# Optimization experiments

Hardware: AMD Instinct MI355X
Metric: run time of the kernel (lower is better)

## Reference

```python
import jax, jax.numpy as jnp
import numpy as np

B, S, D = 2, 2048, 4096
H, HKV, HD = 32, 8, 128
G = H // HKV  # GQA groups
ROPE_BASE = 10000.0


def setup_inputs() -> dict:
    key = jax.random.key(0)
    kx, kq, kk, kv, ko = jax.random.split(key, 5)
    w = 0.02  # init scale for stability
    return {
        "x": jax.random.normal(kx, (B, S, D), dtype=jnp.float32),
        "Wq": jax.random.normal(kq, (D, H * HD), dtype=jnp.float32) * w,
        "Wk": jax.random.normal(kk, (D, HKV * HD), dtype=jnp.float32) * w,
        "Wv": jax.random.normal(kv, (D, HKV * HD), dtype=jnp.float32) * w,
        "Wo": jax.random.normal(ko, (H * HD, D), dtype=jnp.float32) * w,
    }


def _rope(t):
    # t: (B, h, S, HD); rotate-half RoPE, positions = arange(S)
    s = t.shape[2]
    pos = jnp.arange(s, dtype=jnp.float32)
    inv_freq = 1.0 / (ROPE_BASE ** (jnp.arange(0, HD, 2, dtype=jnp.float32) / HD))
    ang = pos[:, None] * inv_freq[None, :]            # (S, HD/2)
    cos = jnp.concatenate([jnp.cos(ang), jnp.cos(ang)], axis=-1)  # (S, HD)
    sin = jnp.concatenate([jnp.sin(ang), jnp.sin(ang)], axis=-1)
    t1, t2 = jnp.split(t, 2, axis=-1)
    rot = jnp.concatenate([-t2, t1], axis=-1)
    return t * cos.astype(t.dtype) + rot * sin.astype(t.dtype)


def reference(x, Wq, Wk, Wv, Wo):
    b, s, _ = x.shape
    q = (x @ Wq).reshape(b, s, H, HD).transpose(0, 2, 1, 3)      # (B,H,S,HD)
    k = (x @ Wk).reshape(b, s, HKV, HD).transpose(0, 2, 1, 3)    # (B,HKV,S,HD)
    v = (x @ Wv).reshape(b, s, HKV, HD).transpose(0, 2, 1, 3)
    q = _rope(q)
    k = _rope(k)
    # GQA: broadcast KV heads across groups instead of repeat_interleave
    qg = q.reshape(b, HKV, G, s, HD)
    scale = 1.0 / jnp.sqrt(jnp.asarray(HD, dtype=x.dtype))
    scores = jnp.einsum('bkgsd,bktd->bkgst', qg, k) * scale       # (B,HKV,G,S,S)
    causal = jnp.tril(jnp.ones((s, s), dtype=bool))
    scores = jnp.where(causal, scores, jnp.finfo(scores.dtype).min)
    p = jax.nn.softmax(scores, axis=-1)
    out = jnp.einsum('bkgst,bktd->bkgsd', p, v)                   # (B,HKV,G,S,HD)
    out = out.reshape(b, H, s, HD).transpose(0, 2, 1, 3).reshape(b, s, H * HD)
    return out @ Wo
```

## Files before the change

kernel.cpp:

```cpp
#include <hip/hip_runtime.h>
#include <hip/hip_bf16.h>

#define B_   2
#define S_   2048
#define D_   4096
#define H_   32
#define HKV_ 8
#define HD_  128
#define QKVS 6144

typedef __bf16 bf16;
typedef __bf16 bf16x8 __attribute__((ext_vector_type(8)));
typedef __bf16 bf16x4 __attribute__((ext_vector_type(4)));
typedef float  f32x4  __attribute__((ext_vector_type(4)));


__global__ void cast_f32_bf16_kernel(const float* __restrict__ in, bf16* __restrict__ out, int n) {
    int i = (blockIdx.x * blockDim.x + threadIdx.x) * 4;
    if (i >= n) return;
    const float4 v = *(const float4*)(in + i);
    bf16x4 o;
    o[0] = (bf16)v.x; o[1] = (bf16)v.y; o[2] = (bf16)v.z; o[3] = (bf16)v.w;
    *(bf16x4*)(out + i) = o;
}

__global__ void transpose_cast_kernel(const float* __restrict__ W, bf16* __restrict__ WT, int K, int N) {
    __shared__ float t[32][33];
    const int n0 = blockIdx.x * 32, k0 = blockIdx.y * 32;
    const int tx = threadIdx.x, ty = threadIdx.y;
    #pragma unroll
    for (int i = ty; i < 32; i += 8) t[i][tx] = W[(size_t)(k0 + i) * N + n0 + tx];
    __syncthreads();
    #pragma unroll
    for (int i = ty; i < 32; i += 8) WT[(size_t)(n0 + i) * K + k0 + tx] = (bf16)t[tx][i];
}

__global__ void transpose_v_kernel(const bf16* __restrict__ V, bf16* __restrict__ Vt) {
    __shared__ bf16 t[32][33];
    const int bh = blockIdx.z;
    const int b = bh >> 3, hk = bh & 7;
    const int d0 = blockIdx.x * 32, s0 = blockIdx.y * 32;
    const int tx = threadIdx.x, ty = threadIdx.y;
    #pragma unroll
    for (int i = ty; i < 32; i += 8)
        t[i][tx] = V[((size_t)(b * S_ + s0 + i)) * QKVS + hk * HD_ + d0 + tx];
    __syncthreads();
    #pragma unroll
    for (int i = ty; i < 32; i += 8)
        Vt[((size_t)(bh * HD_ + d0 + i)) * S_ + s0 + tx] = t[tx][i];
}

__global__ void rope_kernel(bf16* __restrict__ T, int nh, int stride) {
    const int row = blockIdx.x;
    const int pos = row & (S_ - 1);
    const size_t base = (size_t)row * stride;
    const int npairs = nh * 64;
    const float c = 13.287712379549449f / 64.0f;
    for (int p = threadIdx.x; p < npairs; p += blockDim.x) {
        const int h = p >> 6, d = p & 63;
        const float invf = exp2f(-(float)d * c);
        const float ang = (float)pos * invf;
        float sn, cs;
        sincosf(ang, &sn, &cs);
        const size_t i1 = base + (size_t)h * HD_ + d;
        const size_t i2 = i1 + 64;
        const float a  = (float)T[i1];
        const float b2 = (float)T[i2];
        T[i1] = (bf16)(a * cs - b2 * sn);
        T[i2] = (bf16)(b2 * cs + a * sn);
    }
}

__device__ __forceinline__ void gload_lds16(const bf16* g, bf16* l) {
    __builtin_amdgcn_global_load_lds((const __attribute__((address_space(1))) void*)g,
                                     (__attribute__((address_space(3))) void*)l, 16, 0, 0);
}


template <typename CT>
__global__ __launch_bounds__(256) void gemm_bt_kernel(const bf16* __restrict__ A,
                                                      const bf16* __restrict__ Bm,
                                                      CT* __restrict__ C,
                                                      int M, int Cs, int K) {
    __shared__ bf16 As[128 * 32];
    __shared__ bf16 Bs[128 * 32];
    const int m0 = blockIdx.x * 128, n0 = blockIdx.y * 128;
    const int tid = threadIdx.x;
    const int lane = tid & 63, wid = tid >> 6;
    const int wm = wid >> 1, wn = wid & 1;
    const int lg = lane >> 4, lr = lane & 15;
    f32x4 acc[4][4] = {};
    const int arow = tid >> 2;
    const int achunk = (tid & 3) * 8;
    for (int k0 = 0; k0 < K; k0 += 32) {
        gload_lds16(A  + (size_t)(m0 + arow) * K      + k0 + achunk, As + tid * 8);
        gload_lds16(A  + (size_t)(m0 + 64 + arow) * K + k0 + achunk, As + 2048 + tid * 8);
        gload_lds16(Bm + (size_t)(n0 + arow) * K      + k0 + achunk, Bs + tid * 8);
        gload_lds16(Bm + (size_t)(n0 + 64 + arow) * K + k0 + achunk, Bs + 2048 + tid * 8);
        __syncthreads();
        bf16x8 af[4], bfv[4];
        #pragma unroll
        for (int i = 0; i < 4; i++) {
            af[i]  = *(const bf16x8*)(As + (wm * 64 + i * 16 + lr) * 32 + lg * 8);
            bfv[i] = *(const bf16x8*)(Bs + (wn * 64 + i * 16 + lr) * 32 + lg * 8);
        }
        #pragma unroll
        for (int mi = 0; mi < 4; mi++)
            #pragma unroll
            for (int ni = 0; ni < 4; ni++)
                acc[mi][ni] = __builtin_amdgcn_mfma_f32_16x16x32_bf16(af[mi], bfv[ni], acc[mi][ni], 0, 0, 0);
        __syncthreads();
    }
    #pragma unroll
    for (int mi = 0; mi < 4; mi++)
        #pragma unroll
        for (int ni = 0; ni < 4; ni++)
            #pragma unroll
            for (int r = 0; r < 4; r++) {
                const int row = m0 + wm * 64 + mi * 16 + lg * 4 + r;
                const int col = n0 + wn * 64 + ni * 16 + lr;
                C[(size_t)row * Cs + col] = (CT)acc[mi][ni][r];
            }
}


template <typename CT>
__global__ __launch_bounds__(512, 2) void gemm_bt256_kernel(const bf16* __restrict__ A,
                                                            const bf16* __restrict__ Bm,
                                                            CT* __restrict__ C,
                                                            int M, int N, int K, int Cs) {
    __shared__ bf16 sm[65536];
    const int nbx = N >> 8;
    const int cpx = gridDim.x >> 3;
    const int bid = blockIdx.x;
    const int swz = (bid & 7) * cpx + (bid >> 3);
    const int m0 = (swz / nbx) << 8;
    const int n0 = (swz % nbx) << 8;

    const int tid = threadIdx.x;
    const int w = tid >> 6, lane = tid & 63;
    const int wm = w >> 2, wn = w & 3;
    const int lg = lane >> 4, lr = lane & 15;
    const int nkt = K >> 6;

    const bf16* Ab = A + (size_t)m0 * K;
    const bf16* Bb = Bm + (size_t)n0 * K;

    const int u8 = tid >> 3;
    const int schunk = ((tid & 7) ^ (u8 & 7)) << 3;

    auto stageA = [&](int buf, int kt, int h) {
        bf16* dst = sm + buf * 32768 + h * 4096 + tid * 8;
        const bf16* src = Ab + (size_t)(h * 64 + u8) * K + kt * 64 + schunk;
        gload_lds16(src, dst);
        gload_lds16(src + (size_t)128 * K, dst + 8192);
    };
    auto stageB = [&](int buf, int kt, int h) {
        bf16* dst = sm + buf * 32768 + 16384 + h * 2048 + ((u8 >> 5) << 12) + ((u8 & 31) << 6) + ((tid & 7) << 3);
        const bf16* src = Bb + (size_t)(h * 32 + ((u8 >> 5) << 6) + (u8 & 31)) * K + kt * 64 + schunk;
        gload_lds16(src, dst);
        gload_lds16(src + (size_t)128 * K, dst + 8192);
    };

    f32x4 acc[8][4] = {};

    stageA(0, 0, 0); stageA(0, 0, 1); stageB(0, 0, 0); stageB(0, 0, 1);
    stageB(1, 1, 0); stageA(1, 1, 0);
    asm volatile("s_waitcnt vmcnt(4)" ::: "memory");
    __builtin_amdgcn_s_barrier();

    #define MFMA_Q(MI0, NI0, AREG, BREG)                                                     \
        __builtin_amdgcn_s_setprio(1);                                                       \
        _Pragma("unroll") for (int i = 0; i < 4; ++i)                                        \
            _Pragma("unroll") for (int i2 = 0; i2 < 2; ++i2)                                 \
                _Pragma("unroll") for (int kk = 0; kk < 2; ++kk)                             \
                    acc[MI0 + i][NI0 + i2] = __builtin_amdgcn_mfma_f32_16x16x32_bf16(        \
                        AREG[i][kk], BREG[i2][kk], acc[MI0 + i][NI0 + i2], 0, 0, 0);         \
        __builtin_amdgcn_s_setprio(0);                                                       \
        __builtin_amdgcn_s_barrier();

    #define SYNC_IN()                                                                        \
        __builtin_amdgcn_s_barrier();                                                        \
        asm volatile("s_waitcnt lgkmcnt(0)" ::: "memory");                                   \
        __builtin_amdgcn_sched_barrier(0);

    for (int t = 0; t < nkt; ++t) {
        const int cur = t & 1;
        const bf16* curA = sm + cur * 32768;
        const bf16* curB = curA + 16384;
        bf16x8 afc[4][2], b0[2][2], b1[2][2];

        #pragma unroll
        for (int i = 0; i < 4; ++i) {
            const int row = wm * 128 + i * 16 + lr;
            #pragma unroll
            for (int kk = 0; kk < 2; ++kk)
                afc[i][kk] = *(const bf16x8*)(curA + row * 64 + (((kk * 4 + lg) ^ (lr & 7)) << 3));
        }
        #pragma unroll
        for (int i2 = 0; i2 < 2; ++i2) {
            const int row = wn * 64 + i2 * 16 + lr;
            #pragma unroll
            for (int kk = 0; kk < 2; ++kk)
                b0[i2][kk] = *(const bf16x8*)(curB + row * 64 + (((kk * 4 + lg) ^ (lr & 7)) << 3));
        }
        if (t + 1 < nkt) stageA(cur ^ 1, t + 1, 1);
        if (t + 1 == nkt) asm volatile("s_waitcnt vmcnt(0)" ::: "memory");
        SYNC_IN()
        MFMA_Q(0, 0, afc, b0)

        #pragma unroll
        for (int i2 = 0; i2 < 2; ++i2) {
            const int row = wn * 64 + (2 + i2) * 16 + lr;
            #pragma unroll
            for (int kk = 0; kk < 2; ++kk)
                b1[i2][kk] = *(const bf16x8*)(curB + row * 64 + (((kk * 4 + lg) ^ (lr & 7)) << 3));
        }
        if (t + 1 < nkt) stageB(cur ^ 1, t + 1, 1);
        SYNC_IN()
        MFMA_Q(0, 2, afc, b1)

        #pragma unroll
        for (int i = 0; i < 4; ++i) {
            const int row = wm * 128 + (4 + i) * 16 + lr;
            #pragma unroll
            for (int kk = 0; kk < 2; ++kk)
                afc[i][kk] = *(const bf16x8*)(curA + row * 64 + (((kk * 4 + lg) ^ (lr & 7)) << 3));
        }
        if (t + 2 < nkt) stageB(cur, t + 2, 0);
        SYNC_IN()
        MFMA_Q(4, 0, afc, b0)

        if (t + 2 < nkt) stageA(cur, t + 2, 0);
        asm volatile("s_waitcnt vmcnt(4)" ::: "memory");
        SYNC_IN()
        MFMA_Q(4, 2, afc, b1)
    }
    #undef MFMA_Q
    #undef SYNC_IN

    #pragma unroll
    for (int mi = 0; mi < 8; ++mi)
        #pragma unroll
        for (int ni = 0; ni < 4; ++ni)
            #pragma unroll
            for (int r = 0; r < 4; ++r) {
                const int row = m0 + wm * 128 + mi * 16 + lg * 4 + r;
                const int col = n0 + wn * 64 + ni * 16 + lr;
                C[(size_t)row * Cs + col] = (CT)acc[mi][ni][r];
            }
}

#define KVB_ 64

__global__ __launch_bounds__(256) void attn_kernel(const bf16* __restrict__ Q,
                                                   const bf16* __restrict__ Kb,
                                                   const bf16* __restrict__ Vt,
                                                   bf16* __restrict__ O) {
    __shared__ bf16 lds[24576];
    bf16* Ks = lds;
    bf16* Vs = lds + 8192;

    const int flat = blockIdx.x;
    const int x = flat & 7;
    const int j = flat >> 3;
    const int hkb = x * 2 + (j & 1);
    const int qt = 63 - (j >> 1);
    const int hk = hkb & 7, b = hkb >> 3;
    const int q0 = qt * 32;

    const int tid = threadIdx.x;
    const int w = tid >> 6, lane = tid & 63;
    const int lg = lane >> 4, lr = lane & 15;
    const int h = hk * 4 + w;
    bf16* pb = lds + 16384 + w * 2048;

    const bf16* qbase = Q + ((size_t)(b * S_ + q0 + lr)) * QKVS + h * HD_ + lg * 8;
    bf16x8 qf[2][4];
    #pragma unroll
    for (int m = 0; m < 2; m++)
        #pragma unroll
        for (int kk = 0; kk < 4; kk++)
            qf[m][kk] = *(const bf16x8*)(qbase + (size_t)m * 16 * QKVS + kk * 32);

    const bf16* Kh = Kb + ((size_t)b * S_) * QKVS + hk * HD_;
    const bf16* Vh = Vt + ((size_t)(b * HKV_ + hk)) * HD_ * S_;

    const int krow_s  = tid >> 4;
    const int kchnk_s = (tid & 15) ^ (tid >> 4);
    const int vrow_s  = tid >> 3;
    const int vchnk_s = (tid & 7) ^ ((tid >> 3) & 7);

    f32x4 acc[2][8];
    #pragma unroll
    for (int m = 0; m < 2; m++)
        #pragma unroll
        for (int dt = 0; dt < 8; dt++)
            acc[m][dt] = (f32x4){0.f, 0.f, 0.f, 0.f};
    float rowmax[2], rowsum[2];
    #pragma unroll
    for (int m = 0; m < 2; m++) { rowmax[m] = -1e30f; rowsum[m] = 0.f; }

    const float scale = 0.08838834764831845f;
    const int nt = (q0 + 32 + KVB_ - 1) / KVB_;

    for (int it = 0; it < nt; ++it) {
        const int k0 = it * KVB_;
        #pragma unroll
        for (int jj = 0; jj < 4; jj++)
            gload_lds16(Kh + (size_t)(k0 + jj * 16 + krow_s) * QKVS + kchnk_s * 8,
                        Ks + jj * 2048 + tid * 8);
        #pragma unroll
        for (int jj = 0; jj < 4; jj++)
            gload_lds16(Vh + (size_t)(jj * 32 + vrow_s) * S_ + k0 + vchnk_s * 8,
                        Vs + jj * 2048 + tid * 8);
        __syncthreads();

        f32x4 st[2][4];
        #pragma unroll
        for (int m = 0; m < 2; m++)
            #pragma unroll
            for (int kt = 0; kt < 4; kt++)
                st[m][kt] = (f32x4){0.f, 0.f, 0.f, 0.f};
        #pragma unroll
        for (int kt = 0; kt < 4; kt++) {
            bf16x8 kf[4];
            #pragma unroll
            for (int kk = 0; kk < 4; kk++)
                kf[kk] = *(const bf16x8*)(Ks + (kt * 16 + lr) * 128 + (((kk * 4 + lg) ^ lr) << 3));
            #pragma unroll
            for (int m = 0; m < 2; m++)
                #pragma unroll
                for (int kk = 0; kk < 4; kk++)
                    st[m][kt] = __builtin_amdgcn_mfma_f32_16x16x32_bf16(kf[kk], qf[m][kk], st[m][kt], 0, 0, 0);
        }

        const bool need_mask = (k0 + KVB_ - 1 > q0);
        #pragma unroll
        for (int m = 0; m < 2; m++)
            #pragma unroll
            for (int kt = 0; kt < 4; kt++)
                #pragma unroll
                for (int r = 0; r < 4; r++) {
                    float s = st[m][kt][r] * scale;
                    if (need_mask) {
                        const int qg = q0 + m * 16 + lr;
                        const int kg = k0 + kt * 16 + lg * 4 + r;
                        s = (kg <= qg) ? s : -1e30f;
                    }
                    st[m][kt][r] = s;
                }

        float vmax[2];
        #pragma unroll
        for (int m = 0; m < 2; m++) {
            float v = st[m][0][0];
            #pragma unroll
            for (int kt = 0; kt < 4; kt++)
                #pragma unroll
                for (int r = 0; r < 4; r++)
                    v = fmaxf(v, st[m][kt][r]);
            v = fmaxf(v, __shfl_xor(v, 16));
            v = fmaxf(v, __shfl_xor(v, 32));
            vmax[m] = v;
        }
        const bool upd = (vmax[0] > rowmax[0] + 8.0f) || (vmax[1] > rowmax[1] + 8.0f);
        if (__any(upd)) {
            #pragma unroll
            for (int m = 0; m < 2; m++) {
                const float mn = fmaxf(rowmax[m], vmax[m]);
                const float fac = __expf(rowmax[m] - mn);
                rowmax[m] = mn;
                rowsum[m] *= fac;
                #pragma unroll
                for (int r = 0; r < 4; r++) {
                    const float facr = __shfl(fac, lg * 4 + r);
                    #pragma unroll
                    for (int dt = 0; dt < 8; dt++)
                        acc[m][dt][r] *= facr;
                }
            }
        }
        #pragma unroll
        for (int m = 0; m < 2; m++) {
            float ssum = 0.f;
            #pragma unroll
            for (int kt = 0; kt < 4; kt++)
                #pragma unroll
                for (int r = 0; r < 4; r++) {
                    const float pv = __expf(st[m][kt][r] - rowmax[m]);
                    st[m][kt][r] = pv;
                    ssum += pv;
                }
            ssum += __shfl_xor(ssum, 16);
            ssum += __shfl_xor(ssum, 32);
            rowsum[m] += ssum;
        }

        #pragma unroll
        for (int m = 0; m < 2; m++) {
            const int qrow = m * 16 + lr;
            #pragma unroll
            for (int kt = 0; kt < 4; kt++)
                #pragma unroll
                for (int r = 0; r < 4; r++)
                    pb[(qrow * 64 + kt * 16 + lg * 4 + r) ^ ((qrow & 7) << 3)] = (bf16)st[m][kt][r];
        }

        bf16x8 pf[2][2];
        #pragma unroll
        for (int m = 0; m < 2; m++)
            #pragma unroll
            for (int ks = 0; ks < 2; ks++)
                pf[m][ks] = *(const bf16x8*)(pb + (m * 16 + lr) * 64 + ((ks * 32 + lg * 8) ^ ((lr & 7) << 3)));
        #pragma unroll
        for (int dt = 0; dt < 8; dt++) {
            bf16x8 vf[2];
            #pragma unroll
            for (int ks = 0; ks < 2; ks++)
                vf[ks] = *(const bf16x8*)(Vs + (dt * 16 + lr) * 64 + (((ks * 4 + lg) ^ (lr & 7)) << 3));
            #pragma unroll
            for (int m = 0; m < 2; m++)
                #pragma unroll
                for (int ks = 0; ks < 2; ks++)
                    acc[m][dt] = __builtin_amdgcn_mfma_f32_16x16x32_bf16(pf[m][ks], vf[ks], acc[m][dt], 0, 0, 0);
        }
        __syncthreads();
    }

    #pragma unroll
    for (int m = 0; m < 2; m++) {
        float inv[4];
        #pragma unroll
        for (int r = 0; r < 4; r++)
            inv[r] = 1.0f / __shfl(rowsum[m], lg * 4 + r);
        #pragma unroll
        for (int dt = 0; dt < 8; dt++)
            #pragma unroll
            for (int r = 0; r < 4; r++) {
                const size_t row = (size_t)(b * S_ + q0 + m * 16 + lg * 4 + r);
                O[row * (H_ * HD_) + h * HD_ + dt * 16 + lr] = (bf16)(acc[m][dt][r] * inv[r]);
            }
    }
}


extern "C" void kernel_launch(void* const* d_in, const int* in_sizes, int n_in,
                              void* d_out, int out_size, void* d_ws, size_t ws_size,
                              hipStream_t stream) {
    const float* x  = (const float*)d_in[0];
    const float* Wq = (const float*)d_in[1];
    const float* Wk = (const float*)d_in[2];
    const float* Wv = (const float*)d_in[3];
    const float* Wo = (const float*)d_in[4];
    float* out = (float*)d_out;

    const size_t NX   = (size_t)B_ * S_ * D_;
    const size_t NQKVW= (size_t)QKVS * D_;
    const size_t NQKV = (size_t)B_ * S_ * QKVS;
    const size_t NWK  = (size_t)D_ * HKV_ * HD_;

    bf16* p = (bf16*)d_ws;
    bf16* xb    = p;  p += NX;
    bf16* WqkvT = p;  p += NQKVW;
    bf16* QKV   = p;  p += NQKV;
    bf16* Ab  = xb;
    bf16* Vtb = WqkvT;
    bf16* WoT = WqkvT + NWK;

    cast_f32_bf16_kernel<<<(int)(NX / 1024), 256, 0, stream>>>(x, xb, (int)NX);
    transpose_cast_kernel<<<dim3((H_ * HD_) / 32, D_ / 32), dim3(32, 8), 0, stream>>>(Wq, WqkvT, D_, H_ * HD_);
    transpose_cast_kernel<<<dim3((HKV_ * HD_) / 32, D_ / 32), dim3(32, 8), 0, stream>>>(Wk, WqkvT + (size_t)(H_ * HD_) * D_, D_, HKV_ * HD_);
    transpose_cast_kernel<<<dim3((HKV_ * HD_) / 32, D_ / 32), dim3(32, 8), 0, stream>>>(Wv, WqkvT + (size_t)(H_ * HD_ + HKV_ * HD_) * D_, D_, HKV_ * HD_);

    gemm_bt256_kernel<bf16><<<256, 512, 0, stream>>>(xb, WqkvT, QKV, B_ * S_, H_ * HD_, D_, QKVS);
    gemm_bt_kernel<bf16><<<dim3(32, 16), 256, 0, stream>>>(xb, WqkvT + (size_t)(H_ * HD_) * D_,
                                                           QKV + H_ * HD_, B_ * S_, QKVS, D_);

    rope_kernel<<<B_ * S_, 256, 0, stream>>>(QKV, H_ + HKV_, QKVS);

    transpose_v_kernel<<<dim3(HD_ / 32, S_ / 32, B_ * HKV_), dim3(32, 8), 0, stream>>>(QKV + H_ * HD_ + HKV_ * HD_, Vtb);

    attn_kernel<<<1024, 256, 0, stream>>>(QKV, QKV + H_ * HD_, Vtb, Ab);

    transpose_cast_kernel<<<dim3(D_ / 32, (H_ * HD_) / 32), dim3(32, 8), 0, stream>>>(Wo, WoT, H_ * HD_, D_);
    gemm_bt256_kernel<float><<<256, 512, 0, stream>>>(Ab, WoT, out, B_ * S_, D_, H_ * HD_, D_);
}
```

Measured before the change: 601.4 us.

## Switch attention to 32x32x16 MFMA and keep P in registers via lane shuffles

Measured after the change: 591.7 us (median of 2 runs). No clear change (-1.6%).

```diff
diff --git a/kernel.cpp b/kernel.cpp
--- a/kernel.cpp
+++ b/kernel.cpp
@@ -12,7 +12,10 @@
 typedef __bf16 bf16;
 typedef __bf16 bf16x8 __attribute__((ext_vector_type(8)));
 typedef __bf16 bf16x4 __attribute__((ext_vector_type(4)));
+typedef __bf16 bf16x2 __attribute__((ext_vector_type(2)));
 typedef float  f32x4  __attribute__((ext_vector_type(4)));
+typedef float  f32x16 __attribute__((ext_vector_type(16)));
+typedef unsigned int u32x4 __attribute__((ext_vector_type(4)));
 
 
 __global__ void cast_f32_bf16_kernel(const float* __restrict__ in, bf16* __restrict__ out, int n) {
@@ -253,11 +256,16 @@
 
 #define KVB_ 64
 
+__device__ __forceinline__ unsigned int pkbf(float lo, float hi2) {
+    bf16x2 t; t[0] = (bf16)lo; t[1] = (bf16)hi2;
+    return __builtin_bit_cast(unsigned int, t);
+}
+
 __global__ __launch_bounds__(256) void attn_kernel(const bf16* __restrict__ Q,
                                                    const bf16* __restrict__ Kb,
                                                    const bf16* __restrict__ Vt,
                                                    bf16* __restrict__ O) {
-    __shared__ bf16 lds[24576];
+    __shared__ bf16 lds[16384];
     bf16* Ks = lds;
     bf16* Vs = lds + 8192;
 
@@ -271,17 +279,13 @@
 
     const int tid = threadIdx.x;
     const int w = tid >> 6, lane = tid & 63;
-    const int lg = lane >> 4, lr = lane & 15;
+    const int l31 = lane & 31, hi = lane >> 5;
     const int h = hk * 4 + w;
-    bf16* pb = lds + 16384 + w * 2048;
-
-    const bf16* qbase = Q + ((size_t)(b * S_ + q0 + lr)) * QKVS + h * HD_ + lg * 8;
-    bf16x8 qf[2][4];
-    #pragma unroll
-    for (int m = 0; m < 2; m++)
-        #pragma unroll
-        for (int kk = 0; kk < 4; kk++)
-            qf[m][kk] = *(const bf16x8*)(qbase + (size_t)m * 16 * QKVS + kk * 32);
+
+    const bf16* qrow = Q + ((size_t)(b * S_ + q0 + l31)) * QKVS + h * HD_ + hi * 8;
+    bf16x8 qf[8];
+    #pragma unroll
+    for (int t = 0; t < 8; t++) qf[t] = *(const bf16x8*)(qrow + t * 16);
 
     const bf16* Kh = Kb + ((size_t)b * S_) * QKVS + hk * HD_;
     const bf16* Vh = Vt + ((size_t)(b * HKV_ + hk)) * HD_ * S_;
@@ -291,18 +295,14 @@
     const int vrow_s  = tid >> 3;
     const int vchnk_s = (tid & 7) ^ ((tid >> 3) & 7);
 
-    f32x4 acc[2][8];
-    #pragma unroll
-    for (int m = 0; m < 2; m++)
-        #pragma unroll
-        for (int dt = 0; dt < 8; dt++)
-            acc[m][dt] = (f32x4){0.f, 0.f, 0.f, 0.f};
-    float rowmax[2], rowsum[2];
-    #pragma unroll
-    for (int m = 0; m < 2; m++) { rowmax[m] = -1e30f; rowsum[m] = 0.f; }
+    f32x16 acc[4];
+    #pragma unroll
+    for (int dt = 0; dt < 4; dt++) acc[dt] = (f32x16)(0.f);
+    float rowmax = -1e30f, rowsum = 0.f;
 
     const float scale = 0.08838834764831845f;
     const int nt = (q0 + 32 + KVB_ - 1) / KVB_;
+    const int qg = q0 + l31;
 
     for (int it = 0; it < nt; ++it) {
         const int k0 = it * KVB_;
@@ -316,131 +316,104 @@
                         Vs + jj * 2048 + tid * 8);
         __syncthreads();
 
-        f32x4 st[2][4];
-        #pragma unroll
-        for (int m = 0; m < 2; m++)
-            #pragma unroll
-            for (int kt = 0; kt < 4; kt++)
-                st[m][kt] = (f32x4){0.f, 0.f, 0.f, 0.f};
-        #pragma unroll
-        for (int kt = 0; kt < 4; kt++) {
-            bf16x8 kf[4];
-            #pragma unroll
-            for (int kk = 0; kk < 4; kk++)
-                kf[kk] = *(const bf16x8*)(Ks + (kt * 16 + lr) * 128 + (((kk * 4 + lg) ^ lr) << 3));
-            #pragma unroll
-            for (int m = 0; m < 2; m++)
+        f32x16 st0 = (f32x16)(0.f), st1 = (f32x16)(0.f);
+        #pragma unroll
+        for (int t = 0; t < 8; t++) {
+            const int ch = (((2 * t + hi) ^ (l31 & 15)) << 3);
+            const bf16x8 kf0 = *(const bf16x8*)(Ks + l31 * 128 + ch);
+            const bf16x8 kf1 = *(const bf16x8*)(Ks + (32 + l31) * 128 + ch);
+            st0 = __builtin_amdgcn_mfma_f32_32x32x16_bf16(kf0, qf[t], st0, 0, 0, 0);
+            st1 = __builtin_amdgcn_mfma_f32_32x32x16_bf16(kf1, qf[t], st1, 0, 0, 0);
+        }
+
+        const bool need_mask = (k0 + KVB_ - 1 > q0);
+        #pragma unroll
+        for (int r = 0; r < 16; r++) {
+            const int kr = (r & 3) + 8 * (r >> 2) + 4 * hi;
+            float s0 = st0[r] * scale;
+            float s1 = st1[r] * scale;
+            if (need_mask) {
+                s0 = (k0 + kr <= qg) ? s0 : -1e30f;
+                s1 = (k0 + 32 + kr <= qg) ? s1 : -1e30f;
+            }
+            st0[r] = s0; st1[r] = s1;
+        }
+
+        float v = st0[0];
+        #pragma unroll
+        for (int r = 1; r < 16; r++) v = fmaxf(v, st0[r]);
+        #pragma unroll
+        for (int r = 0; r < 16; r++) v = fmaxf(v, st1[r]);
+        v = fmaxf(v, __shfl_xor(v, 32));
+        if (__any(v > rowmax + 8.0f)) {
+            const float mn = fmaxf(rowmax, v);
+            const float fac = __expf(rowmax - mn);
+            rowmax = mn;
+            rowsum *= fac;
+            #pragma unroll
+            for (int r = 0; r < 16; r++) {
+                const float facr = __shfl(fac, (r & 3) + 8 * (r >> 2) + 4 * hi);
                 #pragma unroll
-                for (int kk = 0; kk < 4; kk++)
-                    st[m][kt] = __builtin_amdgcn_mfma_f32_16x16x32_bf16(kf[kk], qf[m][kk], st[m][kt], 0, 0, 0);
-        }
-
-        const bool need_mask = (k0 + KVB_ - 1 > q0);
-        #pragma unroll
-        for (int m = 0; m < 2; m++)
-            #pragma unroll
-            for (int kt = 0; kt < 4; kt++)
-                #pragma unroll
-                for (int r = 0; r < 4; r++) {
-                    float s = st[m][kt][r] * scale;
-                    if (need_mask) {
-                        const int qg = q0 + m * 16 + lr;
-                        const int kg = k0 + kt * 16 + lg * 4 + r;
-                        s = (kg <= qg) ? s : -1e30f;
-                    }
-                    st[m][kt][r] = s;
-                }
-
-        float vmax[2];
-        #pragma unroll
-        for (int m = 0; m < 2; m++) {
-            float v = st[m][0][0];
-            #pragma unroll
-            for (int kt = 0; kt < 4; kt++)
-                #pragma unroll
-                for (int r = 0; r < 4; r++)
-                    v = fmaxf(v, st[m][kt][r]);
-            v = fmaxf(v, __shfl_xor(v, 16));
-            v = fmaxf(v, __shfl_xor(v, 32));
-            vmax[m] = v;
-        }
-        const bool upd = (vmax[0] > rowmax[0] + 8.0f) || (vmax[1] > rowmax[1] + 8.0f);
-        if (__any(upd)) {
-            #pragma unroll
-            for (int m = 0; m < 2; m++) {
-                const float mn = fmaxf(rowmax[m], vmax[m]);
-                const float fac = __expf(rowmax[m] - mn);
-                rowmax[m] = mn;
-                rowsum[m] *= fac;
-                #pragma unroll
-                for (int r = 0; r < 4; r++) {
-                    const float facr = __shfl(fac, lg * 4 + r);
-                    #pragma unroll
-                    for (int dt = 0; dt < 8; dt++)
-                        acc[m][dt][r] *= facr;
-                }
+                for (int dt = 0; dt < 4; dt++) acc[dt][r] *= facr;
             }
         }
-        #pragma unroll
-        for (int m = 0; m < 2; m++) {
-            float ssum = 0.f;
-            #pragma unroll
-            for (int kt = 0; kt < 4; kt++)
-                #pragma unroll
-                for (int r = 0; r < 4; r++) {
-                    const float pv = __expf(st[m][kt][r] - rowmax[m]);
-                    st[m][kt][r] = pv;
-                    ssum += pv;
-                }
-            ssum += __shfl_xor(ssum, 16);
-            ssum += __shfl_xor(ssum, 32);
-            rowsum[m] += ssum;
-        }
-
-        #pragma unroll
-        for (int m = 0; m < 2; m++) {
-            const int qrow = m * 16 + lr;
-            #pragma unroll
-            for (int kt = 0; kt < 4; kt++)
-                #pragma unroll
-                for (int r = 0; r < 4; r++)
-                    pb[(qrow * 64 + kt * 16 + lg * 4 + r) ^ ((qrow & 7) << 3)] = (bf16)st[m][kt][r];
-        }
-
-        bf16x8 pf[2][2];
-        #pragma unroll
-        for (int m = 0; m < 2; m++)
-            #pragma unroll
-            for (int ks = 0; ks < 2; ks++)
-                pf[m][ks] = *(const bf16x8*)(pb + (m * 16 + lr) * 64 + ((ks * 32 + lg * 8) ^ ((lr & 7) << 3)));
-        #pragma unroll
-        for (int dt = 0; dt < 8; dt++) {
-            bf16x8 vf[2];
-            #pragma unroll
-            for (int ks = 0; ks < 2; ks++)
-                vf[ks] = *(const bf16x8*)(Vs + (dt * 16 + lr) * 64 + (((ks * 4 + lg) ^ (lr & 7)) << 3));
-            #pragma unroll
-            for (int m = 0; m < 2; m++)
-                #pragma unroll
-                for (int ks = 0; ks < 2; ks++)
-                    acc[m][dt] = __builtin_amdgcn_mfma_f32_16x16x32_bf16(pf[m][ks], vf[ks], acc[m][dt], 0, 0, 0);
+        float ss = 0.f;
+        #pragma unroll
+        for (int r = 0; r < 16; r++) {
+            const float p0 = __expf(st0[r] - rowmax);
+            const float p1 = __expf(st1[r] - rowmax);
+            st0[r] = p0; st1[r] = p1;
+            ss += p0 + p1;
+        }
+        ss += __shfl_xor(ss, 32);
+        rowsum += ss;
+
+        unsigned int p0k[8], p1k[8];
+        #pragma unroll
+        for (int i = 0; i < 8; i++) {
+            p0k[i] = pkbf(st0[2 * i], st0[2 * i + 1]);
+            p1k[i] = pkbf(st1[2 * i], st1[2 * i + 1]);
+        }
+        bf16x8 pa[4];
+        #pragma unroll
+        for (int kt = 0; kt < 2; kt++) {
+            const unsigned int* pk = kt ? p1k : p0k;
+            const unsigned int sv1 = __shfl_xor((int)(hi ? pk[0] : pk[2]), 32);
+            const unsigned int sv2 = __shfl_xor((int)(hi ? pk[1] : pk[3]), 32);
+            const unsigned int sv3 = __shfl_xor((int)(hi ? pk[4] : pk[6]), 32);
+            const unsigned int sv4 = __shfl_xor((int)(hi ? pk[5] : pk[7]), 32);
+            u32x4 ulo, uhi2;
+            ulo[0] = hi ? sv1 : pk[0];
+            ulo[1] = hi ? sv2 : pk[1];
+            ulo[2] = hi ? pk[2] : sv1;
+            ulo[3] = hi ? pk[3] : sv2;
+            uhi2[0] = hi ? sv3 : pk[4];
+            uhi2[1] = hi ? sv4 : pk[5];
+            uhi2[2] = hi ? pk[6] : sv3;
+            uhi2[3] = hi ? pk[7] : sv4;
+            pa[kt * 2]     = __builtin_bit_cast(bf16x8, ulo);
+            pa[kt * 2 + 1] = __builtin_bit_cast(bf16x8, uhi2);
+        }
+
+        #pragma unroll
+        for (int dt = 0; dt < 4; dt++) {
+            #pragma unroll
+            for (int s = 0; s < 4; s++) {
+                const bf16x8 vf = *(const bf16x8*)(Vs + (dt * 32 + l31) * 64 + (((2 * s + hi) ^ (l31 & 7)) << 3));
+                acc[dt] = __builtin_amdgcn_mfma_f32_32x32x16_bf16(pa[s], vf, acc[dt], 0, 0, 0);
+            }
         }
         __syncthreads();
     }
 
     #pragma unroll
-    for (int m = 0; m < 2; m++) {
-        float inv[4];
-        #pragma unroll
-        for (int r = 0; r < 4; r++)
-            inv[r] = 1.0f / __shfl(rowsum[m], lg * 4 + r);
-        #pragma unroll
-        for (int dt = 0; dt < 8; dt++)
-            #pragma unroll
-            for (int r = 0; r < 4; r++) {
-                const size_t row = (size_t)(b * S_ + q0 + m * 16 + lg * 4 + r);
-                O[row * (H_ * HD_) + h * HD_ + dt * 16 + lr] = (bf16)(acc[m][dt][r] * inv[r]);
-            }
+    for (int r = 0; r < 16; r++) {
+        const int qr = (r & 3) + 8 * (r >> 2) + 4 * hi;
+        const float inv = 1.0f / __shfl(rowsum, qr);
+        bf16* orow = O + ((size_t)(b * S_ + q0 + qr)) * (H_ * HD_) + h * HD_ + l31;
+        #pragma unroll
+        for (int dt = 0; dt < 4; dt++)
+            orow[dt * 32] = (bf16)(acc[dt][r] * inv);
     }
 }
 
```
